# Kernel tuning notes

Hardware: AMD Instinct MI355X
Metric: run time of the kernel (lower is better)

## Reference

```python
import jax, jax.numpy as jnp
import numpy as np

NEG = -1e30  # effective -inf for log-space DP
EPS = 1e-7   # keras backend epsilon used by ctc_batch_cost


def setup_inputs() -> dict:
    key = jax.random.key(0)
    k1, k2 = jax.random.split(key)
    B, T, C, L = 256, 512, 256, 64
    y_true = jax.random.randint(k1, (B, L), 0, C - 1, dtype=jnp.int64)  # labels in [0, C-2]; blank = C-1
    y_pred = jax.random.uniform(k2, (B, T, C), dtype=jnp.float32)       # positive 'probabilities'
    return {"y_true": y_true, "y_pred": y_pred}


def _ctc_batch_cost(y_true, y_pred):
    # Faithful to tf.keras.backend.ctc_batch_cost with input_length=T, label_length=L
    # for every example, blank index = C-1, log applied as log(y_pred + eps).
    B, T, C = y_pred.shape
    L = y_true.shape[1]
    S = 2 * L + 1
    blank = C - 1
    logp = jnp.log(y_pred + EPS)                                  # [B, T, C]

    labels = y_true.astype(jnp.int32)
    # Extended label sequence: blank, l1, blank, l2, ..., lL, blank  -> [B, S]
    ext = jnp.full((B, S), blank, dtype=jnp.int32).at[:, 1::2].set(labels)
    # Skip transition (s-2 -> s) allowed iff s>=2, ext[s] != blank, ext[s] != ext[s-2]
    ext_m2 = jnp.concatenate([jnp.full((B, 2), blank, jnp.int32), ext[:, :-2]], axis=1)
    allow_skip = (jnp.arange(S)[None, :] >= 2) & (ext != blank) & (ext != ext_m2)  # [B, S]

    # Per-time log-probs of extended labels: [B, T, S]
    lp_ext = jnp.take_along_axis(logp, jnp.broadcast_to(ext[:, None, :], (B, T, S)), axis=2)

    # alpha init at t=0: only s=0 (blank) and s=1 (first label) are reachable
    alpha0 = jnp.where(jnp.arange(S)[None, :] < 2, lp_ext[:, 0, :], NEG)  # [B, S]
    neg1 = jnp.full((B, 1), NEG, y_pred.dtype)
    neg2 = jnp.full((B, 2), NEG, y_pred.dtype)

    def step(alpha, lp_t):
        a1 = jnp.concatenate([neg1, alpha[:, :-1]], axis=1)
        a2 = jnp.where(allow_skip, jnp.concatenate([neg2, alpha[:, :-2]], axis=1), NEG)
        m = jnp.maximum(alpha, jnp.maximum(a1, a2))
        new = m + jnp.log(jnp.exp(alpha - m) + jnp.exp(a1 - m) + jnp.exp(a2 - m)) + lp_t
        return new, None

    lp_seq = jnp.transpose(lp_ext[:, 1:, :], (1, 0, 2))            # [T-1, B, S]
    alphaT, _ = jax.lax.scan(step, alpha0, lp_seq)
    loss = -jnp.logaddexp(alphaT[:, S - 1], alphaT[:, S - 2])      # [B]
    return loss[:, None]                                           # [B, 1] like ctc_batch_cost


def reference(y_true, y_pred):
    # CTCLayer.call computes the loss (added via add_loss) and returns y_pred.
    # The loss is the meaningful computation; return it (per-example, [B, 1]).
    return _ctc_batch_cost(y_true, y_pred)
```

## Files before the change

kernel.cpp:

```cpp
#include <hip/hip_runtime.h>


constexpr int Bc = 256;
constexpr int Tc = 512;
constexpr int Cc = 256;
constexpr int Lc = 64;
constexpr int NS = 48;

#define EPSF (1e-7f)
#define NEGF (-1e30f)

__device__ __forceinline__ float flog2(float x) {
    float r; asm("v_log_f32 %0, %1" : "=v"(r) : "v"(x)); return r;
}
__device__ __forceinline__ float fexp2(float x) {
    float r; asm("v_exp_f32 %0, %1" : "=v"(r) : "v"(x)); return r;
}
__device__ __forceinline__ float lse2(float a, float b) {
    float m = fmaxf(a, b);
    float d = fminf(a, b) - m;
    return m + flog2(1.f + fexp2(d));
}
__device__ __forceinline__ float dlog2(double x) {
    if (!(x > 1e-300)) return NEGF;
    const int hb = __double2hiint(x);
    const int lb = __double2loint(x);
    const int e  = ((hb >> 20) & 0x7FF) - 1022;
    const double m = __hiloint2double((hb & 0x800FFFFF) | (1022 << 20), lb);
    return flog2((float)m) + (float)e;
}
__device__ __forceinline__ double dpp_up1_d(double old, double src) {
    const int rl = __builtin_amdgcn_update_dpp(
        __double2loint(old), __double2loint(src), 0x138, 0xF, 0xF, false);
    const int rh = __builtin_amdgcn_update_dpp(
        __double2hiint(old), __double2hiint(src), 0x138, 0xF, 0xF, false);
    return __hiloint2double(rh, rl);
}
__device__ __forceinline__ double dpp_dn1_d(double old, double src) {
    const int rl = __builtin_amdgcn_update_dpp(
        __double2loint(old), __double2loint(src), 0x130, 0xF, 0xF, false);
    const int rh = __builtin_amdgcn_update_dpp(
        __double2hiint(old), __double2hiint(src), 0x130, 0xF, 0xF, false);
    return __hiloint2double(rh, rl);
}

__global__ __launch_bounds__(384, 1) void ctc_fb_kernel(
        const int* __restrict__ y_true,
        const float* __restrict__ y_pred,
        float* __restrict__ out)
{
    const int b    = blockIdx.x;
    const int lane = threadIdx.x & 63;
    const int wid  = threadIdx.x >> 6;

    __shared__ float ring[2][NS][Cc];
    __shared__ float Cl[64], Ch[64];
    __shared__ float CexS;

    const float* __restrict__ bbase = y_pred + (size_t)b * Tc * Cc;

    double lo = 0.0, hi = 0.0, ex = 0.0;

    if (wid >= 2) {
        const int pid  = wid - 2;
        const int dir  = pid & 1;
        const int half = pid >> 1;
        const float* __restrict__ g0 =
            dir ? (bbase + (size_t)(Tc - 1) * Cc + lane * 4)
                : (bbase + lane * 4);
        const ptrdiff_t stp = dir ? -(ptrdiff_t)Cc : (ptrdiff_t)Cc;

        float4 a0, a1, a2, a3, b0, b1, b2, b3;

#define GADDR(G, j) (g0 + stp * (8 * (G) + 4 * half + (j)))
#define LADDR(G, j) (&ring[dir][((G) % 6) * 8 + 4 * half + (j)][lane * 4])
#define PLOAD(v0, v1, v2, v3, G)                                   \
        v0 = *(const float4*)GADDR(G, 0);                          \
        v1 = *(const float4*)GADDR(G, 1);                          \
        v2 = *(const float4*)GADDR(G, 2);                          \
        v3 = *(const float4*)GADDR(G, 3);
#define PWRITE(v0, v1, v2, v3, G)                                  \
        *(float4*)LADDR(G, 0) = v0;                                \
        *(float4*)LADDR(G, 1) = v1;                                \
        *(float4*)LADDR(G, 2) = v2;                                \
        *(float4*)LADDR(G, 3) = v3;

        PLOAD(a0, a1, a2, a3, 0)
        PLOAD(b0, b1, b2, b3, 1)
        asm volatile("s_waitcnt vmcnt(4)" ::: "memory");
        PWRITE(a0, a1, a2, a3, 0)
        asm volatile("s_waitcnt lgkmcnt(0)" ::: "memory");

        for (int g = 0; g < 32; g += 2) {
            asm volatile("" ::: "memory");
            __builtin_amdgcn_s_barrier();
            asm volatile("" ::: "memory");
            if (g + 2 <= 31) { PLOAD(a0, a1, a2, a3, g + 2) }
            if (g <= 29) asm volatile("s_waitcnt vmcnt(4)" ::: "memory");
            else         asm volatile("s_waitcnt vmcnt(0)" ::: "memory");
            PWRITE(b0, b1, b2, b3, g + 1)
            asm volatile("s_waitcnt lgkmcnt(0)" ::: "memory");
            asm volatile("" ::: "memory");
            __builtin_amdgcn_s_barrier();
            asm volatile("" ::: "memory");
            if (g + 3 <= 31) { PLOAD(b0, b1, b2, b3, g + 3) }
            if (g + 1 <= 29) asm volatile("s_waitcnt vmcnt(4)" ::: "memory");
            else             asm volatile("s_waitcnt vmcnt(0)" ::: "memory");
            if (g + 2 <= 31) {
                PWRITE(a0, a1, a2, a3, g + 2)
                asm volatile("s_waitcnt lgkmcnt(0)" ::: "memory");
            }
        }
#undef GADDR
#undef LADDR
#undef PLOAD
#undef PWRITE
    } else {
        const int lab  = y_true[b * Lc + lane];
        const int labp = __shfl_up(lab, 1);
        const int labn = __shfl_down(lab, 1);

        if (wid == 0) {
            const bool allowF = (lane >= 1) && (lab != labp);
            auto stepF = [&](float pBf, float pLf) {
                const double pB = (double)pBf, pL = (double)pLf;
                const double prevHi = dpp_up1_d(0.0, hi);
                const double sk  = allowF ? prevHi : 0.0;
                const double nlo = (lo + prevHi) * pB;
                const double nhi = (hi + lo + sk) * pL;
                ex = (ex + hi) * pB;
                hi = nhi; lo = nlo;
            };
            int sb = 0;
            for (int g = 0; g < 32; ++g) {
                asm volatile("" ::: "memory");
                __builtin_amdgcn_s_barrier();
                asm volatile("" ::: "memory");
#define RDF(j) const float cL##j = ring[0][sb + j][lab] + EPSF, \
                           cB##j = ring[0][sb + j][Cc - 1] + EPSF;
                RDF(0) RDF(1) RDF(2) RDF(3) RDF(4) RDF(5) RDF(6) RDF(7)
#undef RDF
                if (g == 0) {
                    lo = (lane == 0) ? (double)cB0 : 0.0;
                    hi = (lane == 0) ? (double)cL0 : 0.0;
                } else stepF(cB0, cL0);
                stepF(cB1, cL1); stepF(cB2, cL2); stepF(cB3, cL3);
                stepF(cB4, cL4); stepF(cB5, cL5); stepF(cB6, cL6);
                stepF(cB7, cL7);
                sb += 8; if (sb >= NS) sb = 0;
            }
        } else {
            const bool allowB = (lane < 63) && (labn != lab);
            auto stepB = [&](float pBf, float pLf) {
                const double pB = (double)pBf, pL = (double)pLf;
                const double nlo_s = dpp_dn1_d(ex, lo);
                const double nhi_s = dpp_dn1_d(0.0, hi);
                const double sk = allowB ? nhi_s : 0.0;
                const double l2 = (lo + hi) * pB;
                const double h2 = (hi + nlo_s + sk) * pL;
                ex = ex * pB;
                lo = l2; hi = h2;
            };
            int sb = 0;
            for (int g = 0; g < 32; ++g) {
                asm volatile("" ::: "memory");
                __builtin_amdgcn_s_barrier();
                asm volatile("" ::: "memory");
#define RDB(j) const float cL##j = ring[1][sb + j][lab] + EPSF, \
                           cB##j = ring[1][sb + j][Cc - 1] + EPSF;
                RDB(0) RDB(1) RDB(2) RDB(3) RDB(4) RDB(5) RDB(6) RDB(7)
#undef RDB
                if (g == 0) {
                    ex = (double)cB0;
                    hi = (lane == 63) ? (double)cL0 : 0.0;
                    lo = 0.0;
                } else stepB(cB0, cL0);
                stepB(cB1, cL1); stepB(cB2, cL2); stepB(cB3, cL3);
                stepB(cB4, cL4); stepB(cB5, cL5); stepB(cB6, cL6);
                stepB(cB7, cL7);
                sb += 8; if (sb >= NS) sb = 0;
            }
            const double nlo_s = dpp_dn1_d(ex, lo);
            const double nhi_s = dpp_dn1_d(0.0, hi);
            const double sk = allowB ? nhi_s : 0.0;
            Cl[lane] = dlog2(lo + hi);
            Ch[lane] = dlog2(hi + nlo_s + sk);
            if (lane == 63) CexS = dlog2(ex);
        }
    }

    __syncthreads();

    if (wid == 0) {
        const float w1 = dlog2(lo) + Cl[lane];
        const float w2 = dlog2(hi) + Ch[lane];
        float w = lse2(w1, w2);
        if (lane == 63) w = lse2(w, dlog2(ex) + CexS);
        #pragma unroll
        for (int off = 32; off; off >>= 1) w = lse2(w, __shfl_xor(w, off));
        if (lane == 0)
            out[b] = -0.69314718055994530942f * w;
    }
}

extern "C" void kernel_launch(void* const* d_in, const int* in_sizes, int n_in,
                              void* d_out, int out_size, void* d_ws, size_t ws_size,
                              hipStream_t stream) {
    const int*   y_true = (const int*)d_in[0];
    const float* y_pred = (const float*)d_in[1];
    float*       out    = (float*)d_out;
    ctc_fb_kernel<<<dim3(Bc), dim3(384), 0, stream>>>(y_true, y_pred, out);
}
```

Before: 25.29 us.

## Replace block-wide barriers with per-slot LDS flags between producer and consumer waves

```diff
diff --git a/kernel.cpp b/kernel.cpp
--- a/kernel.cpp
+++ b/kernel.cpp
@@ -5,7 +5,7 @@
 constexpr int Tc = 512;
 constexpr int Cc = 256;
 constexpr int Lc = 64;
-constexpr int NS = 48;
+constexpr int NG = 8;
 
 #define EPSF (1e-7f)
 #define NEGF (-1e30f)
@@ -53,9 +53,17 @@
     const int lane = threadIdx.x & 63;
     const int wid  = threadIdx.x >> 6;
 
-    __shared__ float ring[2][NS][Cc];
+    __shared__ float ring[2][NG * 8][Cc];
+    __shared__ volatile int pflag[2][2][NG];
+    __shared__ volatile int cdone[2];
     __shared__ float Cl[64], Ch[64];
     __shared__ float CexS;
+
+    if (threadIdx.x < 32)
+        pflag[threadIdx.x >> 4][(threadIdx.x >> 3) & 1][threadIdx.x & 7] = -1;
+    if (threadIdx.x == 32) cdone[0] = -1;
+    if (threadIdx.x == 33) cdone[1] = -1;
+    __syncthreads();
 
     const float* __restrict__ bbase = y_pred + (size_t)b * Tc * Cc;
 
@@ -73,7 +81,7 @@
         float4 a0, a1, a2, a3, b0, b1, b2, b3;
 
 #define GADDR(G, j) (g0 + stp * (8 * (G) + 4 * half + (j)))
-#define LADDR(G, j) (&ring[dir][((G) % 6) * 8 + 4 * half + (j)][lane * 4])
+#define LADDR(G, j) (&ring[dir][((G) & 7) * 8 + 4 * half + (j)][lane * 4])
 #define PLOAD(v0, v1, v2, v3, G)                                   \
         v0 = *(const float4*)GADDR(G, 0);                          \
         v1 = *(const float4*)GADDR(G, 1);                          \
@@ -84,37 +92,34 @@
         *(float4*)LADDR(G, 1) = v1;                                \
         *(float4*)LADDR(G, 2) = v2;                                \
         *(float4*)LADDR(G, 3) = v3;
+#define GUARD(G)                                                   \
+        if ((G) >= NG) { while (cdone[dir] < (G) - NG) {} }        \
+        asm volatile("" ::: "memory");
+#define FLAG(G)                                                    \
+        asm volatile("s_waitcnt lgkmcnt(0)" ::: "memory");         \
+        pflag[dir][half][(G) & 7] = (G);
 
         PLOAD(a0, a1, a2, a3, 0)
-        PLOAD(b0, b1, b2, b3, 1)
-        asm volatile("s_waitcnt vmcnt(4)" ::: "memory");
-        PWRITE(a0, a1, a2, a3, 0)
-        asm volatile("s_waitcnt lgkmcnt(0)" ::: "memory");
-
         for (int g = 0; g < 32; g += 2) {
-            asm volatile("" ::: "memory");
-            __builtin_amdgcn_s_barrier();
-            asm volatile("" ::: "memory");
+            if (g + 1 <= 31) { PLOAD(b0, b1, b2, b3, g + 1) }
+            if (g + 1 <= 31) asm volatile("s_waitcnt vmcnt(4)" ::: "memory");
+            else             asm volatile("s_waitcnt vmcnt(0)" ::: "memory");
+            GUARD(g)
+            PWRITE(a0, a1, a2, a3, g)
+            FLAG(g)
             if (g + 2 <= 31) { PLOAD(a0, a1, a2, a3, g + 2) }
-            if (g <= 29) asm volatile("s_waitcnt vmcnt(4)" ::: "memory");
-            else         asm volatile("s_waitcnt vmcnt(0)" ::: "memory");
+            if (g + 2 <= 31) asm volatile("s_waitcnt vmcnt(4)" ::: "memory");
+            else             asm volatile("s_waitcnt vmcnt(0)" ::: "memory");
+            GUARD(g + 1)
             PWRITE(b0, b1, b2, b3, g + 1)
-            asm volatile("s_waitcnt lgkmcnt(0)" ::: "memory");
-            asm volatile("" ::: "memory");
-            __builtin_amdgcn_s_barrier();
-            asm volatile("" ::: "memory");
-            if (g + 3 <= 31) { PLOAD(b0, b1, b2, b3, g + 3) }
-            if (g + 1 <= 29) asm volatile("s_waitcnt vmcnt(4)" ::: "memory");
-            else             asm volatile("s_waitcnt vmcnt(0)" ::: "memory");
-            if (g + 2 <= 31) {
-                PWRITE(a0, a1, a2, a3, g + 2)
-                asm volatile("s_waitcnt lgkmcnt(0)" ::: "memory");
-            }
+            FLAG(g + 1)
         }
 #undef GADDR
 #undef LADDR
 #undef PLOAD
 #undef PWRITE
+#undef GUARD
+#undef FLAG
     } else {
         const int lab  = y_true[b * Lc + lane];
         const int labp = __shfl_up(lab, 1);
@@ -131,11 +136,10 @@
                 ex = (ex + hi) * pB;
                 hi = nhi; lo = nlo;
             };
-            int sb = 0;
             for (int g = 0; g < 32; ++g) {
+                while (pflag[0][0][g & 7] < g || pflag[0][1][g & 7] < g) {}
                 asm volatile("" ::: "memory");
-                __builtin_amdgcn_s_barrier();
-                asm volatile("" ::: "memory");
+                const int sb = (g & 7) * 8;
 #define RDF(j) const float cL##j = ring[0][sb + j][lab] + EPSF, \
                            cB##j = ring[0][sb + j][Cc - 1] + EPSF;
                 RDF(0) RDF(1) RDF(2) RDF(3) RDF(4) RDF(5) RDF(6) RDF(7)
@@ -147,7 +151,8 @@
                 stepF(cB1, cL1); stepF(cB2, cL2); stepF(cB3, cL3);
                 stepF(cB4, cL4); stepF(cB5, cL5); stepF(cB6, cL6);
                 stepF(cB7, cL7);
-                sb += 8; if (sb >= NS) sb = 0;
+                asm volatile("s_waitcnt lgkmcnt(0)" ::: "memory");
+                cdone[0] = g;
             }
         } else {
             const bool allowB = (lane < 63) && (labn != lab);
@@ -161,11 +166,10 @@
                 ex = ex * pB;
                 lo = l2; hi = h2;
             };
-            int sb = 0;
             for (int g = 0; g < 32; ++g) {
+                while (pflag[1][0][g & 7] < g || pflag[1][1][g & 7] < g) {}
                 asm volatile("" ::: "memory");
-                __builtin_amdgcn_s_barrier();
-                asm volatile("" ::: "memory");
+                const int sb = (g & 7) * 8;
 #define RDB(j) const float cL##j = ring[1][sb + j][lab] + EPSF, \
                            cB##j = ring[1][sb + j][Cc - 1] + EPSF;
                 RDB(0) RDB(1) RDB(2) RDB(3) RDB(4) RDB(5) RDB(6) RDB(7)
@@ -178,7 +182,8 @@
                 stepB(cB1, cL1); stepB(cB2, cL2); stepB(cB3, cL3);
                 stepB(cB4, cL4); stepB(cB5, cL5); stepB(cB6, cL6);
                 stepB(cB7, cL7);
-                sb += 8; if (sb >= NS) sb = 0;
+                asm volatile("s_waitcnt lgkmcnt(0)" ::: "memory");
+                cdone[1] = g;
             }
             const double nlo_s = dpp_dn1_d(ex, lo);
             const double nhi_s = dpp_dn1_d(0.0, hi);
```

Measured after the change: 27.12 us. +7.2%, slower.

## Split forward and backward CTC passes into separate blocks joined via atomic flag

Applied to the files above, without the earlier changes.

```diff
diff --git a/kernel.cpp b/kernel.cpp
--- a/kernel.cpp
+++ b/kernel.cpp
@@ -9,6 +9,8 @@
 
 #define EPSF (1e-7f)
 #define NEGF (-1e30f)
+#define WS_VEC_OFF 1024
+#define VSTRIDE 132
 
 __device__ __forceinline__ float flog2(float x) {
     float r; asm("v_log_f32 %0, %1" : "=v"(r) : "v"(x)); return r;
@@ -44,27 +46,25 @@
     return __hiloint2double(rh, rl);
 }
 
-__global__ __launch_bounds__(384, 1) void ctc_fb_kernel(
+__global__ __launch_bounds__(192, 1) void ctc_half_kernel(
         const int* __restrict__ y_true,
         const float* __restrict__ y_pred,
-        float* __restrict__ out)
+        float* __restrict__ out,
+        float* __restrict__ wsv,
+        int*   __restrict__ flags)
 {
-    const int b    = blockIdx.x;
+    const int bid  = blockIdx.x;
+    const int b    = bid & 255;
+    const int dir  = bid >> 8;
     const int lane = threadIdx.x & 63;
     const int wid  = threadIdx.x >> 6;
 
-    __shared__ float ring[2][NS][Cc];
-    __shared__ float Cl[64], Ch[64];
-    __shared__ float CexS;
+    __shared__ float ring[NS][Cc];
 
     const float* __restrict__ bbase = y_pred + (size_t)b * Tc * Cc;
 
-    double lo = 0.0, hi = 0.0, ex = 0.0;
-
-    if (wid >= 2) {
-        const int pid  = wid - 2;
-        const int dir  = pid & 1;
-        const int half = pid >> 1;
+    if (wid >= 1) {
+        const int half = wid - 1;
         const float* __restrict__ g0 =
             dir ? (bbase + (size_t)(Tc - 1) * Cc + lane * 4)
                 : (bbase + lane * 4);
@@ -73,7 +73,7 @@
         float4 a0, a1, a2, a3, b0, b1, b2, b3;
 
 #define GADDR(G, j) (g0 + stp * (8 * (G) + 4 * half + (j)))
-#define LADDR(G, j) (&ring[dir][((G) % 6) * 8 + 4 * half + (j)][lane * 4])
+#define LADDR(G, j) (&ring[((G) % 6) * 8 + 4 * half + (j)][lane * 4])
 #define PLOAD(v0, v1, v2, v3, G)                                   \
         v0 = *(const float4*)GADDR(G, 0);                          \
         v1 = *(const float4*)GADDR(G, 1);                          \
@@ -115,87 +115,102 @@
 #undef LADDR
 #undef PLOAD
 #undef PWRITE
+        return;
+    }
+
+    const int lab  = y_true[b * Lc + lane];
+    const int labp = __shfl_up(lab, 1);
+    const int labn = __shfl_down(lab, 1);
+
+    double lo = 0.0, hi = 0.0, ex = 0.0;
+    float v1, v2, v3;
+
+    if (dir == 0) {
+        const bool allowF = (lane >= 1) && (lab != labp);
+        auto stepF = [&](float pBf, float pLf) {
+            const double pB = (double)pBf, pL = (double)pLf;
+            const double prevHi = dpp_up1_d(0.0, hi);
+            const double sk  = allowF ? prevHi : 0.0;
+            const double nlo = (lo + prevHi) * pB;
+            const double nhi = (hi + lo + sk) * pL;
+            ex = (ex + hi) * pB;
+            hi = nhi; lo = nlo;
+        };
+        int sb = 0;
+        for (int g = 0; g < 32; ++g) {
+            asm volatile("" ::: "memory");
+            __builtin_amdgcn_s_barrier();
+            asm volatile("" ::: "memory");
+#define RDF(j) const float cL##j = ring[sb + j][lab] + EPSF, \
+                           cB##j = ring[sb + j][Cc - 1] + EPSF;
+            RDF(0) RDF(1) RDF(2) RDF(3) RDF(4) RDF(5) RDF(6) RDF(7)
+#undef RDF
+            if (g == 0) {
+                lo = (lane == 0) ? (double)cB0 : 0.0;
+                hi = (lane == 0) ? (double)cL0 : 0.0;
+            } else stepF(cB0, cL0);
+            stepF(cB1, cL1); stepF(cB2, cL2); stepF(cB3, cL3);
+            stepF(cB4, cL4); stepF(cB5, cL5); stepF(cB6, cL6);
+            stepF(cB7, cL7);
+            sb += 8; if (sb >= NS) sb = 0;
+        }
+        v1 = dlog2(lo); v2 = dlog2(hi); v3 = dlog2(ex);
     } else {
-        const int lab  = y_true[b * Lc + lane];
-        const int labp = __shfl_up(lab, 1);
-        const int labn = __shfl_down(lab, 1);
-
-        if (wid == 0) {
-            const bool allowF = (lane >= 1) && (lab != labp);
-            auto stepF = [&](float pBf, float pLf) {
-                const double pB = (double)pBf, pL = (double)pLf;
-                const double prevHi = dpp_up1_d(0.0, hi);
-                const double sk  = allowF ? prevHi : 0.0;
-                const double nlo = (lo + prevHi) * pB;
-                const double nhi = (hi + lo + sk) * pL;
-                ex = (ex + hi) * pB;
-                hi = nhi; lo = nlo;
-            };
-            int sb = 0;
-            for (int g = 0; g < 32; ++g) {
-                asm volatile("" ::: "memory");
-                __builtin_amdgcn_s_barrier();
-                asm volatile("" ::: "memory");
-#define RDF(j) const float cL##j = ring[0][sb + j][lab] + EPSF, \
-                           cB##j = ring[0][sb + j][Cc - 1] + EPSF;
-                RDF(0) RDF(1) RDF(2) RDF(3) RDF(4) RDF(5) RDF(6) RDF(7)
-#undef RDF
-                if (g == 0) {
-                    lo = (lane == 0) ? (double)cB0 : 0.0;
-                    hi = (lane == 0) ? (double)cL0 : 0.0;
-                } else stepF(cB0, cL0);
-                stepF(cB1, cL1); stepF(cB2, cL2); stepF(cB3, cL3);
-                stepF(cB4, cL4); stepF(cB5, cL5); stepF(cB6, cL6);
-                stepF(cB7, cL7);
-                sb += 8; if (sb >= NS) sb = 0;
-            }
-        } else {
-            const bool allowB = (lane < 63) && (labn != lab);
-            auto stepB = [&](float pBf, float pLf) {
-                const double pB = (double)pBf, pL = (double)pLf;
-                const double nlo_s = dpp_dn1_d(ex, lo);
-                const double nhi_s = dpp_dn1_d(0.0, hi);
-                const double sk = allowB ? nhi_s : 0.0;
-                const double l2 = (lo + hi) * pB;
-                const double h2 = (hi + nlo_s + sk) * pL;
-                ex = ex * pB;
-                lo = l2; hi = h2;
-            };
-            int sb = 0;
-            for (int g = 0; g < 32; ++g) {
-                asm volatile("" ::: "memory");
-                __builtin_amdgcn_s_barrier();
-                asm volatile("" ::: "memory");
-#define RDB(j) const float cL##j = ring[1][sb + j][lab] + EPSF, \
-                           cB##j = ring[1][sb + j][Cc - 1] + EPSF;
-                RDB(0) RDB(1) RDB(2) RDB(3) RDB(4) RDB(5) RDB(6) RDB(7)
-#undef RDB
-                if (g == 0) {
-                    ex = (double)cB0;
-                    hi = (lane == 63) ? (double)cL0 : 0.0;
-                    lo = 0.0;
-                } else stepB(cB0, cL0);
-                stepB(cB1, cL1); stepB(cB2, cL2); stepB(cB3, cL3);
-                stepB(cB4, cL4); stepB(cB5, cL5); stepB(cB6, cL6);
-                stepB(cB7, cL7);
-                sb += 8; if (sb >= NS) sb = 0;
-            }
+        const bool allowB = (lane < 63) && (labn != lab);
+        auto stepB = [&](float pBf, float pLf) {
+            const double pB = (double)pBf, pL = (double)pLf;
             const double nlo_s = dpp_dn1_d(ex, lo);
             const double nhi_s = dpp_dn1_d(0.0, hi);
             const double sk = allowB ? nhi_s : 0.0;
-            Cl[lane] = dlog2(lo + hi);
-            Ch[lane] = dlog2(hi + nlo_s + sk);
-            if (lane == 63) CexS = dlog2(ex);
+            const double l2 = (lo + hi) * pB;
+            const double h2 = (hi + nlo_s + sk) * pL;
+            ex = ex * pB;
+            lo = l2; hi = h2;
+        };
+        int sb = 0;
+        for (int g = 0; g < 32; ++g) {
+            asm volatile("" ::: "memory");
+            __builtin_amdgcn_s_barrier();
+            asm volatile("" ::: "memory");
+#define RDB(j) const float cL##j = ring[sb + j][lab] + EPSF, \
+                           cB##j = ring[sb + j][Cc - 1] + EPSF;
+            RDB(0) RDB(1) RDB(2) RDB(3) RDB(4) RDB(5) RDB(6) RDB(7)
+#undef RDB
+            if (g == 0) {
+                ex = (double)cB0;
+                hi = (lane == 63) ? (double)cL0 : 0.0;
+                lo = 0.0;
+            } else stepB(cB0, cL0);
+            stepB(cB1, cL1); stepB(cB2, cL2); stepB(cB3, cL3);
+            stepB(cB4, cL4); stepB(cB5, cL5); stepB(cB6, cL6);
+            stepB(cB7, cL7);
+            sb += 8; if (sb >= NS) sb = 0;
         }
+        const double nlo_s = dpp_dn1_d(ex, lo);
+        const double nhi_s = dpp_dn1_d(0.0, hi);
+        const double sk = allowB ? nhi_s : 0.0;
+        v1 = dlog2(lo + hi);
+        v2 = dlog2(hi + nlo_s + sk);
+        v3 = dlog2(ex);
     }
 
-    __syncthreads();
-
-    if (wid == 0) {
-        const float w1 = dlog2(lo) + Cl[lane];
-        const float w2 = dlog2(hi) + Ch[lane];
+    float* myv = wsv + (size_t)(((dir << 8) | b) * VSTRIDE);
+    myv[lane]      = v1;
+    myv[64 + lane] = v2;
+    if (lane == 63) myv[128] = v3;
+    __threadfence();
+    int old = 0;
+    if (lane == 0) old = atomicAdd(&flags[b], 1);
+    old = __shfl(old, 0);
+    if (old == 1) {
+        __threadfence();
+        asm volatile("" ::: "memory");
+        volatile const float* A = wsv + (size_t)(b * VSTRIDE);
+        volatile const float* C = wsv + (size_t)((256 + b) * VSTRIDE);
+        const float w1 = A[lane]      + C[lane];
+        const float w2 = A[64 + lane] + C[64 + lane];
         float w = lse2(w1, w2);
-        if (lane == 63) w = lse2(w, dlog2(ex) + CexS);
+        if (lane == 63) w = lse2(w, A[128] + C[128]);
         #pragma unroll
         for (int off = 32; off; off >>= 1) w = lse2(w, __shfl_xor(w, off));
         if (lane == 0)
@@ -209,5 +224,9 @@
     const int*   y_true = (const int*)d_in[0];
     const float* y_pred = (const float*)d_in[1];
     float*       out    = (float*)d_out;
-    ctc_fb_kernel<<<dim3(Bc), dim3(384), 0, stream>>>(y_true, y_pred, out);
-}
+    int*         flags  = (int*)d_ws;
+    float*       wsv    = (float*)((char*)d_ws + WS_VEC_OFF);
+    hipMemsetAsync(d_ws, 0, WS_VEC_OFF, stream);
+    ctc_half_kernel<<<dim3(2 * Bc), dim3(192), 0, stream>>>(
+        y_true, y_pred, out, wsv, flags);
+}
```

After: 47.97 us. 89.6% more time.
